# Optimization experiments

Hardware: AMD Instinct MI355X
Metric: run time of the kernel (lower is better)

## Reference

```python
import jax, jax.numpy as jnp
import numpy as np

# ---- module hyper-params (match init_kwargs) ----
B, C_IN, C_OUT, K, H, W = 16, 128, 128, 3, 56, 56
M, G, STRIDE, RED = 2, 2, 1, 16
R = max(RED, C_IN // RED)            # GC_Attention bottleneck width = 16
MO = M * C_OUT                       # gc_att output channels
GROUPS = G * C_OUT                   # grouped 1x1 fc groups = 256
IN_PG = MO // GROUPS                 # in channels per group = M // G = 1
COUT_FC = C_OUT * C_IN * K * K       # generated weight elements per sample
OUT_PG = COUT_FC // GROUPS           # out channels per group = 576
PAD = K // 2
LN_EPS = 1e-5


def setup_inputs() -> dict:
    key = jax.random.key(0)
    ks = jax.random.split(key, 6)
    sc = 0.05
    return {
        "x": jax.random.normal(ks[0], (B, C_IN, H, W), jnp.float32),
        # GC_Attention: conv_mask (1x1, C->1)
        "w_mask": jax.random.normal(ks[1], (C_IN,), jnp.float32) * sc,
        "b_mask": jnp.zeros((), jnp.float32),
        # transform: conv1x1 C->R, LayerNorm(R), ReLU, conv1x1 R->M*out
        "w1": jax.random.normal(ks[2], (R, C_IN), jnp.float32) * sc,
        "b1": jnp.zeros((R,), jnp.float32),
        "ln_g": jnp.ones((R,), jnp.float32),
        "ln_b": jnp.zeros((R,), jnp.float32),
        "w2": jax.random.normal(ks[3], (MO, R), jnp.float32) * sc,
        "b2": jnp.zeros((MO,), jnp.float32),
        # fc: grouped 1x1 conv, groups=G*out, stored [groups, out_pg, in_pg]
        "w_fc": jax.random.normal(ks[4], (GROUPS, OUT_PG, IN_PG), jnp.float32) * sc,
        "b_fc": jnp.zeros((COUT_FC,), jnp.float32),
    }


def reference(x, w_mask, b_mask, w1, b1, ln_g, ln_b, w2, b2, w_fc, b_fc):
    b, c, h, w = x.shape
    # --- GC_Attention: global-context pooling via spatial softmax ---
    mask = jnp.einsum('bchw,c->bhw', x, w_mask) + b_mask        # [b,h,w]
    att = jax.nn.softmax(mask.reshape(b, -1), axis=-1)          # [b,hw]
    ctx = jnp.einsum('bcs,bs->bc', x.reshape(b, c, -1), att)    # [b,C]
    # bottleneck transform (1x1 convs on [b,*,1,1] == dense layers)
    t = ctx @ w1.T + b1                                          # [b,R]
    mu = t.mean(-1, keepdims=True)
    var = t.var(-1, keepdims=True)
    t = (t - mu) / jnp.sqrt(var + LN_EPS) * ln_g + ln_b          # LayerNorm over R
    t = jax.nn.relu(t)
    a = jax.nn.sigmoid(t @ w2.T + b2)                            # [b, M*out]
    # --- grouped 1x1 conv: generate per-sample conv weights ---
    xw = jnp.einsum('bgi,goi->bgo', a.reshape(b, GROUPS, IN_PG), w_fc)
    xw = xw.reshape(b, COUT_FC) + b_fc
    Wd = xw.reshape(b, C_OUT, C_IN, K, K)                        # per-sample kernels
    # --- per-sample conv2d (torch: groups=b on batch-folded input) ---
    def conv1(xi, wi):
        return jax.lax.conv_general_dilated(
            xi[None], wi, (STRIDE, STRIDE), [(PAD, PAD), (PAD, PAD)],
            dimension_numbers=('NCHW', 'OIHW', 'NCHW'))[0]
    return jax.vmap(conv1)(x, Wd)                                # [b, out, H, W]
```

## Files before the change

kernel.cpp:

```cpp
#include <hip/hip_runtime.h>
#include <hip/hip_bf16.h>
#include <math.h>

#define BATCH 16
#define CIN   128
#define COUT  128
#define SS    3136
#define XT_ROW 8192
#define XT_PER_B (58*XT_ROW)
#define NKB   18

typedef __attribute__((ext_vector_type(8))) __bf16 bf16x8;
typedef __attribute__((ext_vector_type(4))) float  floatx4;

static __device__ __forceinline__ unsigned short f2bf(float f) {
  union { float f; unsigned u; } v; v.f = f;
  unsigned r = v.u + 0x7fffu + ((v.u >> 16) & 1u);
  return (unsigned short)(r >> 16);
}
static __device__ __forceinline__ float bf2f(unsigned short u) {
  union { unsigned u; float f; } v; v.u = ((unsigned)u) << 16; return v.f;
}

static __device__ __forceinline__ float waveReduceSum(float v) {
  #pragma unroll
  for (int off = 32; off > 0; off >>= 1) v += __shfl_xor(v, off, 64);
  return v;
}

static __device__ __forceinline__ void load_lds16(const void* g, void* l) {
  __builtin_amdgcn_global_load_lds(
      (const __attribute__((address_space(1))) void*)g,
      (__attribute__((address_space(3))) void*)l, 16, 0, 0);
}

__global__ void k0_padT(const float* __restrict__ x, const float* __restrict__ w_mask,
                        const float* __restrict__ b_mask,
                        unsigned short* __restrict__ xT, float* __restrict__ rowsum,
                        float* __restrict__ pctx) {
  int b = blockIdx.y, prow = blockIdx.x, t = threadIdx.x;
  int y = prow - 1;
  __shared__ unsigned short sx[128 * 58];
  __shared__ float swm[128];
  __shared__ float red[4 * 56];
  __shared__ float se[56];
  bool rowvalid = ((unsigned)y < 56u);
  if (t < 128) swm[t] = w_mask[t];
  if (rowvalid) {
    int ci = t >> 1, h = t & 1;
    const float* src = x + (size_t)(b * 128 + ci) * SS + y * 56 + h * 28;
    #pragma unroll
    for (int c = 0; c < 28; c++) sx[ci * 58 + h * 28 + c] = f2bf(src[c]);
  } else {
    for (int i = t; i < 128 * 58; i += 256) sx[i] = 0;
  }
  __syncthreads();
  if (rowvalid && t < 224) {
    int xx = t % 56, g = t / 56;
    float acc = 0.f;
    #pragma unroll
    for (int k = 0; k < 32; k++) {
      int ci = g * 32 + k;
      acc += bf2f(sx[ci * 58 + xx]) * swm[ci];
    }
    red[g * 56 + xx] = acc;
  }
  __syncthreads();
  float e = 0.f;
  if (rowvalid && t < 56) {
    float m = red[t] + red[56 + t] + red[112 + t] + red[168 + t] + b_mask[0];
    e = expf(m);
    se[t] = e;
  }
  if (t < 64) {
    float s = waveReduceSum(e);
    if (t == 0) rowsum[b * 58 + prow] = s;
  }
  __syncthreads();
  {
    int c = t >> 1, h = t & 1;
    float acc = 0.f;
    if (rowvalid) {
      #pragma unroll
      for (int j = 0; j < 28; j++)
        acc += bf2f(sx[c * 58 + h * 28 + j]) * se[h * 28 + j];
    }
    acc += __shfl_xor(acc, 1, 64);
    if (h == 0) pctx[(size_t)(b * 58 + prow) * 128 + c] = acc;
  }
  int pcol = t >> 2, cig = t & 3;
  int xx = pcol - 1;
  bool colv = rowvalid && ((unsigned)xx < 56u);
  unsigned short tmp[32];
  #pragma unroll
  for (int i = 0; i < 32; i++)
    tmp[i] = colv ? sx[(cig * 32 + i) * 58 + xx] : (unsigned short)0;
  unsigned short* dst = xT + ((size_t)(b * 58 + prow) * 64 + pcol) * 128 + cig * 32;
  #pragma unroll
  for (int q = 0; q < 4; q++)
    *reinterpret_cast<uint4*>(dst + q * 8) = *reinterpret_cast<const uint4*>(tmp + q * 8);
}

__global__ void k5_gen(const float* __restrict__ rowsum, const float* __restrict__ pctx,
                       const float* __restrict__ w1, const float* __restrict__ b1,
                       const float* __restrict__ ln_g, const float* __restrict__ ln_b,
                       const float* __restrict__ w2, const float* __restrict__ b2,
                       const float* __restrict__ w_fc, const float* __restrict__ b_fc,
                       unsigned short* __restrict__ wd) {
  int co = blockIdx.x, b = blockIdx.y, t = threadIdx.x;
  __shared__ float sc[128], st[16], sn[16], sa[2], shz;
  float rv = (t < 58) ? rowsum[b * 58 + t] : 0.f;
  float acc = 0.f;
  #pragma unroll
  for (int r = 0; r < 58; r++) acc += pctx[(size_t)(b * 58 + r) * 128 + t];
  if (t < 64) {
    float z = waveReduceSum(rv);
    if (t == 0) shz = 1.0f / z;
  }
  __syncthreads();
  sc[t] = acc * shz;
  __syncthreads();
  if (t < 16) {
    float s = b1[t];
    #pragma unroll 8
    for (int c = 0; c < 128; c++) s += sc[c] * w1[t * 128 + c];
    st[t] = s;
  }
  __syncthreads();
  float mu = 0.f, m2 = 0.f;
  #pragma unroll
  for (int r = 0; r < 16; r++) { float v = st[r]; mu += v; m2 += v * v; }
  mu *= (1.f / 16.f); m2 *= (1.f / 16.f);
  float rstd = rsqrtf(m2 - mu * mu + 1e-5f);
  if (t < 16) {
    float v = (st[t] - mu) * rstd * ln_g[t] + ln_b[t];
    sn[t] = fmaxf(v, 0.f);
  }
  __syncthreads();
  if (t < 2) {
    int mo = 2 * co + t;
    float s = b2[mo];
    #pragma unroll
    for (int r = 0; r < 16; r++) s += sn[r] * w2[mo * 16 + r];
    sa[t] = 1.f / (1.f + expf(-s));
  }
  __syncthreads();
  float a0 = sa[0], a1 = sa[1];
  const float* wrow = w_fc + co * 1152;
  const float* brow = b_fc + co * 1152;
  unsigned short* drow = wd + (size_t)(b * 128 + co) * 1152;
  #pragma unroll
  for (int r = 0; r < 9; r++) {
    int e = t + 128 * r;
    int ci = e / 9, khw = e - (e / 9) * 9;
    float v = (ci < 64 ? a0 : a1) * wrow[e] + brow[e];
    int kb = khw * 2 + (ci >> 6);
    int kq = ci & 63;
    int pos = (((kq >> 3) ^ (co & 7)) << 3) | (kq & 7);
    drow[kb * 64 + pos] = f2bf(v);
  }
}

__global__ __launch_bounds__(512, 4) void k6_conv(const unsigned short* __restrict__ xT,
                                                  const unsigned short* __restrict__ wd,
                                                  float* __restrict__ out) {
  __shared__ __align__(16) unsigned short As[8192];
  __shared__ __align__(16) unsigned short Bs[8192];
  int t = threadIdx.x;
  int b = blockIdx.y, y0 = blockIdx.x * 2;
  int wave = t >> 6, lane = t & 63, l15 = lane & 15, quad = lane >> 4;
  int x7 = lane & 7;
  const unsigned short* wp  = wd + (size_t)b * (128 * 1152);
  const unsigned short* xTb = xT + (size_t)b * XT_PER_B;

  int ch0 = wave * 128 + lane, ch1 = ch0 + 64;
  int offA0 = (ch0 >> 3) * 1152 + (ch0 & 7) * 8;
  int offA1 = (ch1 >> 3) * 1152 + (ch1 & 7) * 8;
  int s0 = ch0 >> 3, s1 = ch1 >> 3;
  int c_ = lane & 7;
  int sr0 = s0 / 56, sc0 = s0 - sr0 * 56; if (sr0 >= 2) { sr0 = 0; sc0 = 0; }
  int sr1 = s1 / 56, sc1 = s1 - sr1 * 56; if (sr1 >= 2) { sr1 = 0; sc1 = 0; }
  int offB0 = (y0 + sr0) * XT_ROW + sc0 * 128 + (c_ ^ (s0 & 7)) * 8;
  int offB1 = (y0 + sr1) * XT_ROW + sc1 * 128 + (c_ ^ (s1 & 7)) * 8;
  unsigned short* dA0 = &As[wave * 1024];
  unsigned short* dA1 = &As[wave * 1024 + 512];
  unsigned short* dB0 = &Bs[wave * 1024];
  unsigned short* dB1 = &Bs[wave * 1024 + 512];

  int s_base = (wave & 3) * 32;
  int co_b   = (wave >> 2) * 64;

  floatx4 acc[4][2];
  floatx4 zero = {0.f, 0.f, 0.f, 0.f};
  #pragma unroll
  for (int i = 0; i < 4; i++)
    #pragma unroll
    for (int j = 0; j < 2; j++) acc[i][j] = zero;

  for (int kb = 0; kb < NKB; kb++) {
    int khw = kb >> 1;
    int kh = khw / 3;
    int kw = khw - kh * 3;
    int dB = kh * XT_ROW + kw * 128 + ((kb & 1) << 6);
    int dA = kb * 64;
    __syncthreads();
    load_lds16(wp + offA0 + dA, dA0);
    load_lds16(wp + offA1 + dA, dA1);
    load_lds16(xTb + offB0 + dB, dB0);
    load_lds16(xTb + offB1 + dB, dB1);
    __syncthreads();
    #pragma unroll
    for (int kk = 0; kk < 2; kk++) {
      bf16x8 af[4], bfr[2];
      int pc = ((kk * 4 + quad) ^ x7) << 3;
      #pragma unroll
      for (int i = 0; i < 4; i++)
        af[i] = *reinterpret_cast<const bf16x8*>(&As[(co_b + i * 16 + l15) * 64 + pc]);
      #pragma unroll
      for (int j = 0; j < 2; j++)
        bfr[j] = *reinterpret_cast<const bf16x8*>(&Bs[(s_base + j * 16 + l15) * 64 + pc]);
      #pragma unroll
      for (int i = 0; i < 4; i++)
        #pragma unroll
        for (int j = 0; j < 2; j++)
          acc[i][j] = __builtin_amdgcn_mfma_f32_16x16x32_bf16(af[i], bfr[j], acc[i][j], 0, 0, 0);
    }
  }

  float* ob = out + (size_t)b * COUT * SS + y0 * 56;
  #pragma unroll
  for (int i = 0; i < 4; i++) {
    #pragma unroll
    for (int j = 0; j < 2; j++) {
      int sl = s_base + j * 16 + l15;
      if (sl < 112) {
        int row = (sl >= 56) ? 1 : 0;
        int col = sl - row * 56;
        #pragma unroll
        for (int r = 0; r < 4; r++) {
          int co = co_b + i * 16 + quad * 4 + r;
          ob[(size_t)co * SS + row * 56 + col] = acc[i][j][r];
        }
      }
    }
  }
}

extern "C" void kernel_launch(void* const* d_in, const int* in_sizes, int n_in,
                              void* d_out, int out_size, void* d_ws, size_t ws_size,
                              hipStream_t stream) {
  const float* x      = (const float*)d_in[0];
  const float* w_mask = (const float*)d_in[1];
  const float* b_mask = (const float*)d_in[2];
  const float* w1     = (const float*)d_in[3];
  const float* b1     = (const float*)d_in[4];
  const float* ln_g   = (const float*)d_in[5];
  const float* ln_b   = (const float*)d_in[6];
  const float* w2     = (const float*)d_in[7];
  const float* b2     = (const float*)d_in[8];
  const float* w_fc   = (const float*)d_in[9];
  const float* b_fc   = (const float*)d_in[10];
  float* out = (float*)d_out;

  char* ws = (char*)d_ws;
  unsigned short* xT  = (unsigned short*)(ws);
  unsigned short* wdw = (unsigned short*)(ws + 15204352);
  float* rowsum = (float*)(ws + 19922944);
  float* pctx   = (float*)(ws + 19927040);

  k0_padT<<<dim3(58, 16),  dim3(256), 0, stream>>>(x, w_mask, b_mask, xT, rowsum, pctx);
  k5_gen <<<dim3(128, 16), dim3(128), 0, stream>>>(rowsum, pctx, w1, b1, ln_g, ln_b,
                                                   w2, b2, w_fc, b_fc, wdw);
  k6_conv<<<dim3(28, 16),  dim3(512), 0, stream>>>(xT, wdw, out);
}
```

Measured before the change: 134.0 us.

## Stage full 4-row input halo in LDS once per conv block instead of per-tap reloads

```diff
diff --git a/kernel.cpp b/kernel.cpp
--- a/kernel.cpp
+++ b/kernel.cpp
@@ -48,9 +48,16 @@
   if (t < 128) swm[t] = w_mask[t];
   if (rowvalid) {
     int ci = t >> 1, h = t & 1;
-    const float* src = x + (size_t)(b * 128 + ci) * SS + y * 56 + h * 28;
-    #pragma unroll
-    for (int c = 0; c < 28; c++) sx[ci * 58 + h * 28 + c] = f2bf(src[c]);
+    const float4* src = (const float4*)(x + (size_t)(b * 128 + ci) * SS + y * 56 + h * 28);
+    #pragma unroll
+    for (int c4 = 0; c4 < 7; c4++) {
+      float4 v = src[c4];
+      int base = ci * 58 + h * 28 + c4 * 4;
+      sx[base]     = f2bf(v.x);
+      sx[base + 1] = f2bf(v.y);
+      sx[base + 2] = f2bf(v.z);
+      sx[base + 3] = f2bf(v.w);
+    }
   } else {
     for (int i = t; i < 128 * 58; i += 256) sx[i] = 0;
   }
@@ -165,31 +172,42 @@
                                                   const unsigned short* __restrict__ wd,
                                                   float* __restrict__ out) {
   __shared__ __align__(16) unsigned short As[8192];
-  __shared__ __align__(16) unsigned short Bs[8192];
+  __shared__ __align__(16) unsigned short Bs[32768];
   int t = threadIdx.x;
   int b = blockIdx.y, y0 = blockIdx.x * 2;
   int wave = t >> 6, lane = t & 63, l15 = lane & 15, quad = lane >> 4;
   int x7 = lane & 7;
   const unsigned short* wp  = wd + (size_t)b * (128 * 1152);
-  const unsigned short* xTb = xT + (size_t)b * XT_PER_B;
-
-  int ch0 = wave * 128 + lane, ch1 = ch0 + 64;
-  int offA0 = (ch0 >> 3) * 1152 + (ch0 & 7) * 8;
+  const unsigned short* xTb = xT + (size_t)b * XT_PER_B + (size_t)y0 * XT_ROW;
+
+  #pragma unroll
+  for (int i = 0; i < 8; i++) {
+    int g = i * 512 + t;
+    int row  = g >> 10;
+    int pcol = (g >> 4) & 63;
+    int c    = g & 15;
+    int csrc = (c & 8) | ((c & 7) ^ (pcol & 7));
+    load_lds16(xTb + (size_t)((row * 64 + pcol) * 16 + csrc) * 8,
+               &Bs[(size_t)(i * 512 + wave * 64) * 8]);
+  }
+
+  int offA0 = (t >> 3) * 1152 + (t & 7) * 8;
+  int ch1 = t + 512;
   int offA1 = (ch1 >> 3) * 1152 + (ch1 & 7) * 8;
-  int s0 = ch0 >> 3, s1 = ch1 >> 3;
-  int c_ = lane & 7;
-  int sr0 = s0 / 56, sc0 = s0 - sr0 * 56; if (sr0 >= 2) { sr0 = 0; sc0 = 0; }
-  int sr1 = s1 / 56, sc1 = s1 - sr1 * 56; if (sr1 >= 2) { sr1 = 0; sc1 = 0; }
-  int offB0 = (y0 + sr0) * XT_ROW + sc0 * 128 + (c_ ^ (s0 & 7)) * 8;
-  int offB1 = (y0 + sr1) * XT_ROW + sc1 * 128 + (c_ ^ (s1 & 7)) * 8;
-  unsigned short* dA0 = &As[wave * 1024];
-  unsigned short* dA1 = &As[wave * 1024 + 512];
-  unsigned short* dB0 = &Bs[wave * 1024];
-  unsigned short* dB1 = &Bs[wave * 1024 + 512];
 
   int s_base = (wave & 3) * 32;
   int co_b   = (wave >> 2) * 64;
 
+  int srw[2], scl[2];
+  #pragma unroll
+  for (int j = 0; j < 2; j++) {
+    int s = s_base + j * 16 + l15;
+    int r = (s >= 56) ? 1 : 0;
+    int cc = s - r * 56;
+    if (s >= 112) { r = 0; cc = s - 112; }
+    srw[j] = r; scl[j] = cc;
+  }
+
   floatx4 acc[4][2];
   floatx4 zero = {0.f, 0.f, 0.f, 0.f};
   #pragma unroll
@@ -197,28 +215,29 @@
     #pragma unroll
     for (int j = 0; j < 2; j++) acc[i][j] = zero;
 
+  #pragma unroll 1
   for (int kb = 0; kb < NKB; kb++) {
     int khw = kb >> 1;
     int kh = khw / 3;
     int kw = khw - kh * 3;
-    int dB = kh * XT_ROW + kw * 128 + ((kb & 1) << 6);
-    int dA = kb * 64;
     __syncthreads();
-    load_lds16(wp + offA0 + dA, dA0);
-    load_lds16(wp + offA1 + dA, dA1);
-    load_lds16(xTb + offB0 + dB, dB0);
-    load_lds16(xTb + offB1 + dB, dB1);
+    load_lds16(wp + offA0 + kb * 64, &As[wave * 512]);
+    load_lds16(wp + offA1 + kb * 64, &As[4096 + wave * 512]);
     __syncthreads();
     #pragma unroll
     for (int kk = 0; kk < 2; kk++) {
       bf16x8 af[4], bfr[2];
-      int pc = ((kk * 4 + quad) ^ x7) << 3;
+      int pcA = ((kk * 4 + quad) ^ x7) << 3;
       #pragma unroll
       for (int i = 0; i < 4; i++)
-        af[i] = *reinterpret_cast<const bf16x8*>(&As[(co_b + i * 16 + l15) * 64 + pc]);
-      #pragma unroll
-      for (int j = 0; j < 2; j++)
-        bfr[j] = *reinterpret_cast<const bf16x8*>(&Bs[(s_base + j * 16 + l15) * 64 + pc]);
+        af[i] = *reinterpret_cast<const bf16x8*>(&As[(co_b + i * 16 + l15) * 64 + pcA]);
+      int c = ((kb & 1) << 3) + kk * 4 + quad;
+      #pragma unroll
+      for (int j = 0; j < 2; j++) {
+        int pq = scl[j] + kw;
+        int cs = (c & 8) | ((c & 7) ^ (pq & 7));
+        bfr[j] = *reinterpret_cast<const bf16x8*>(&Bs[(((srw[j] + kh) * 64 + pq) * 16 + cs) * 8]);
+      }
       #pragma unroll
       for (int i = 0; i < 4; i++)
         #pragma unroll
```

After: 136.9 us. 2.2% more time.
